# Optimization experiments

Measured on AMD Instinct MI355X. Metric: run time of the kernel, lower is better.

## Reference

```python
import jax, jax.numpy as jnp
import numpy as np

N, D = 768, 128  # num_cells, gnn embedding dim (sum(gnn_layers_out_chnls))

def setup_inputs() -> dict:
    key = jax.random.key(0)
    ks = jax.random.split(key, 5)
    z = jax.random.normal(ks[0], (N, D), dtype=jnp.float32)
    W1 = jax.random.normal(ks[1], (256, 2 * D), dtype=jnp.float32) * 0.05
    b1 = jnp.zeros((256,), dtype=jnp.float32)
    W2 = jax.random.normal(ks[2], (128, 256), dtype=jnp.float32) * 0.05
    b2 = jnp.zeros((128,), dtype=jnp.float32)
    Wf = jax.random.normal(ks[3], (2, 128), dtype=jnp.float32) * 0.05
    bf = jnp.zeros((2,), dtype=jnp.float32)
    return {"z": z, "W1": W1, "b1": b1, "W2": W2, "b2": b2, "Wf": Wf, "bf": bf}

def reference(z, W1, b1, W2, b2, Wf, bf):
    # pairs[i, j] = concat(z[j], z[i])  (rtile varies over j, ctile over i)
    # First 1x1 conv over the 2D-channel pair tensor is equivalent to two
    # small matmuls broadcast-summed (same math, avoids N*N*2D materialization).
    d = z.shape[1]
    row_part = jnp.einsum('jd,od->jo', z, W1[:, :d])   # contribution of z[j]
    col_part = jnp.einsum('id,od->io', z, W1[:, d:])   # contribution of z[i]
    h = jax.nn.relu(row_part[None, :, :] + col_part[:, None, :] + b1)  # [N, N, 256]
    # dropout is identity in eval mode (training=False)
    h = jax.nn.relu(jnp.einsum('ijc,oc->ijo', h, W2) + b2)             # [N, N, 128]
    dists = jnp.einsum('ijc,oc->ijo', h, Wf) + bf                      # [N, N, 2]
    return dists
```

## Files before the change

### kernel.cpp

```cpp
#include <hip/hip_runtime.h>


typedef __attribute__((ext_vector_type(8)))  _Float16     f16x8;
typedef __attribute__((ext_vector_type(2)))  float        f32x2;
typedef __attribute__((ext_vector_type(4)))  float        f32x4;
typedef __attribute__((ext_vector_type(16))) float        f32x16;

#define NCELL 768
#define DIM   128
#define C1    256
#define C2    128

#define CPB    0
#define CB     1024
#define WFT    3072
#define B2T    4096
#define LDS_SZ 4608

static __device__ __forceinline__ f32x2 pk_add(f32x2 a, f32x2 b) {
    f32x2 d; asm("v_pk_add_f32 %0, %1, %2" : "=v"(d) : "v"(a), "v"(b)); return d;
}
static __device__ __forceinline__ f32x2 pk_fma(f32x2 a, f32x2 b, f32x2 c) {
    f32x2 d; asm("v_pk_fma_f32 %0, %1, %2, %3" : "=v"(d) : "v"(a), "v"(b), "v"(c)); return d;
}
static __device__ __forceinline__ f32x2 relu2(f32x2 a) {
    f32x2 d; d[0] = fmaxf(a[0], 0.f); d[1] = fmaxf(a[1], 0.f); return d;
}
static __device__ __forceinline__ f32x2 lo2(f32x4 v) { return __builtin_shufflevector(v, v, 0, 1); }
static __device__ __forceinline__ f32x2 hi2(f32x4 v) { return __builtin_shufflevector(v, v, 2, 3); }

__global__ __launch_bounds__(256) void prep_all(const float* __restrict__ z,
                                                const float* __restrict__ W1,
                                                const float* __restrict__ b1,
                                                const float* __restrict__ W2,
                                                _Float16* __restrict__ rp16,
                                                _Float16* __restrict__ cp16,
                                                _Float16* __restrict__ w2h) {
    const int tid = threadIdx.x;
    if (blockIdx.x < 192) {
        const int jb4 = blockIdx.x * 4;
        __shared__ float zl[4 * DIM];
        zl[tid]       = z[(size_t)jb4 * DIM + tid];
        zl[tid + 256] = z[(size_t)jb4 * DIM + tid + 256];
        __syncthreads();
        const int o = tid;
        float a1[4] = {0.f, 0.f, 0.f, 0.f};
        float a2[4] = {0.f, 0.f, 0.f, 0.f};
        const f32x4* w4 = (const f32x4*)(W1 + (size_t)o * (2 * DIM));
#pragma unroll 4
        for (int d4 = 0; d4 < 32; ++d4) {
            f32x4 wa = w4[d4], wb = w4[32 + d4];
#pragma unroll
            for (int jj = 0; jj < 4; ++jj) {
                f32x4 zv = *(const f32x4*)(zl + jj * DIM + d4 * 4);
#pragma unroll
                for (int e = 0; e < 4; ++e) {
                    a1[jj] = fmaf(zv[e], wa[e], a1[jj]);
                    a2[jj] = fmaf(zv[e], wb[e], a2[jj]);
                }
            }
        }
        const float bb = b1[o];
#pragma unroll
        for (int jj = 0; jj < 4; ++jj) {
            rp16[(size_t)(jb4 + jj) * C1 + o] = (_Float16)(a1[jj] + bb);
            cp16[(size_t)(jb4 + jj) * C1 + o] = (_Float16)a2[jj];
        }
    } else {
        const int t = (blockIdx.x - 192) * 256 + tid;
        w2h[t] = (_Float16)W2[t];
    }
}

__global__ __launch_bounds__(256, 2) void pair_head(const _Float16* __restrict__ rp16,
                                                    const _Float16* __restrict__ cp16,
                                                    const _Float16* __restrict__ w2h,
                                                    const float* __restrict__ Wf,
                                                    const float* __restrict__ b2,
                                                    const float* __restrict__ bfv,
                                                    float* __restrict__ out) {
    __shared__ char smem[LDS_SZ];
    const int tid = threadIdx.x;
    const int nh  = tid >> 6;
    const int l   = tid & 63;
    const int ln  = l & 31;
    const int kh  = l >> 5;
    const int jbg = blockIdx.x >> 6;
    const int ic  = blockIdx.x & 63;
    const int j0  = jbg * 32;
    const int i_base = ic * 12;

    if (tid < 128) {
        int idx = tid >> 1, o = tid & 1;
        int kk = idx >> 5, q = (idx >> 2) & 7, ng = idx & 3;
        int r = 2 * q;
        int n0 = ng * 32 + (r & 3) + 8 * (r >> 2) + 4 * kk;
        f32x2 e = {Wf[o * C2 + n0], Wf[o * C2 + n0 + 1]};
        *(f32x2*)(smem + WFT + idx * 16 + o * 8) = e;
    }
    if (tid < 64) {
        int idx = tid;
        int kk = idx >> 5, q = (idx >> 2) & 7, ng = idx & 3;
        int r = 2 * q;
        int n0 = ng * 32 + (r & 3) + 8 * (r >> 2) + 4 * kk;
        f32x2 e = {b2[n0], b2[n0 + 1]};
        *(f32x2*)(smem + B2T + idx * 8) = e;
    }
    if (tid < 128) {
        unsigned v = *(const unsigned*)((const char*)cp16 + (size_t)i_base * 512 + tid * 4);
        *(unsigned*)(smem + CPB + tid * 4) = v;
    }

    f16x8 rpf[16];
    {
        const char* rsrc = (const char*)rp16 + (size_t)(j0 + ln) * 512 + kh * 16;
#pragma unroll
        for (int ks = 0; ks < 16; ++ks)
            rpf[ks] = *(const f16x8*)(rsrc + ks * 32);
    }
    f16x8 w2f[16];
#pragma unroll
    for (int ks = 0; ks < 16; ++ks)
        w2f[ks] = *(const f16x8*)(w2h + (size_t)(nh * 32 + ln) * C1 + ks * 16 + kh * 8);

    __syncthreads();

    const float bf0 = bfv[0], bf1 = bfv[1];
    const f16x8 zero8 = (f16x8)(_Float16)0.0f;

    for (int t = 0; t < 12; ++t) {
        unsigned cpv = 0;
        if (t < 11 && tid < 128)
            cpv = *(const unsigned*)((const char*)cp16 + (size_t)(i_base + t + 1) * 512 + tid * 4);

        const char* cbbase = smem + CPB + (t & 1) * 512 + kh * 16;

        f32x16 acc = (f32x16)0.f;
#pragma unroll
        for (int ks = 0; ks < 16; ++ks) {
            f16x8 cv = *(const f16x8*)(cbbase + ks * 32);
            f16x8 hb = __builtin_elementwise_max(rpf[ks] + cv, zero8);
            acc = __builtin_amdgcn_mfma_f32_32x32x16_f16(w2f[ks], hb, acc, 0, 0, 0);
        }

        f32x2 P0 = {0.f, 0.f}, P1 = {0.f, 0.f};
#pragma unroll
        for (int q = 0; q < 8; ++q) {
            int idx = kh * 32 + q * 4 + nh;
            f32x4 w01 = *(const f32x4*)(smem + WFT + idx * 16);
            f32x2 bb  = *(const f32x2*)(smem + B2T + idx * 8);
            f32x2 s = {acc[2 * q], acc[2 * q + 1]};
            s = relu2(pk_add(s, bb));
            P0 = pk_fma(lo2(w01), s, P0);
            P1 = pk_fma(hi2(w01), s, P1);
        }
        float p0 = P0[0] + P0[1], p1 = P1[0] + P1[1];
        p0 += __shfl_xor(p0, 32);
        p1 += __shfl_xor(p1, 32);
        if (kh == 0)
            *(f32x2*)(smem + CB + (t & 1) * 1024 + nh * 256 + ln * 8) = (f32x2){p0, p1};

        if (t < 11 && tid < 128)
            *(unsigned*)(smem + CPB + ((t + 1) & 1) * 512 + tid * 4) = cpv;

        __syncthreads();

        if (nh == (t & 3) && kh == 0) {
            const char* cbse = smem + CB + (t & 1) * 1024 + ln * 8;
            f32x2 a0 = *(const f32x2*)(cbse);
            f32x2 a1 = *(const f32x2*)(cbse + 256);
            f32x2 a2 = *(const f32x2*)(cbse + 512);
            f32x2 a3 = *(const f32x2*)(cbse + 768);
            float o0 = a0[0] + a1[0] + a2[0] + a3[0] + bf0;
            float o1 = a0[1] + a1[1] + a2[1] + a3[1] + bf1;
            const int i = i_base + t;
            *(f32x2*)(out + ((size_t)i * NCELL + j0 + ln) * 2) = (f32x2){o0, o1};
        }
    }
}

extern "C" void kernel_launch(void* const* d_in, const int* in_sizes, int n_in,
                              void* d_out, int out_size, void* d_ws, size_t ws_size,
                              hipStream_t stream) {
    const float* z   = (const float*)d_in[0];
    const float* W1  = (const float*)d_in[1];
    const float* b1  = (const float*)d_in[2];
    const float* W2  = (const float*)d_in[3];
    const float* b2  = (const float*)d_in[4];
    const float* Wf  = (const float*)d_in[5];
    const float* bfv = (const float*)d_in[6];
    float* out = (float*)d_out;

    _Float16* rp16 = (_Float16*)d_ws;
    _Float16* cp16 = rp16 + NCELL * C1;
    _Float16* w2h  = cp16 + NCELL * C1;

    prep_all<<<192 + 128, 256, 0, stream>>>(z, W1, b1, W2, rp16, cp16, w2h);
    pair_head<<<24 * 64, 256, 0, stream>>>(rp16, cp16, w2h, Wf, b2, bfv, out);
}
```

Baseline: 77.13 us.

## Switch pair head to 16x16x32 MFMA tiles with batched epilogue and single sync

Replaces the 32x32x16 MFMA per i-row with 16x16x32 MFMAs that process two i rows and two j halves at once, reusing each W2 and rp fragment across four products. The full block of 12 cp rows is staged into LDS up front, so the per-iteration double-buffered prefetch and the per-iteration __syncthreads go away. The Wf/b2 tables are packed into one table, and output reduction is deferred to a single pass after the loop. The cost is more accumulator registers and a larger LDS footprint, which could reduce occupancy.

Measured after the change: 64.04 us. 17.0% less time.

```diff
diff --git a/kernel.cpp b/kernel.cpp
--- a/kernel.cpp
+++ b/kernel.cpp
@@ -1,33 +1,21 @@
 #include <hip/hip_runtime.h>
 
 
-typedef __attribute__((ext_vector_type(8)))  _Float16     f16x8;
-typedef __attribute__((ext_vector_type(2)))  float        f32x2;
-typedef __attribute__((ext_vector_type(4)))  float        f32x4;
-typedef __attribute__((ext_vector_type(16))) float        f32x16;
+typedef __attribute__((ext_vector_type(8)))  _Float16 f16x8;
+typedef __attribute__((ext_vector_type(2)))  float    f32x2;
+typedef __attribute__((ext_vector_type(4)))  float    f32x4;
 
 #define NCELL 768
 #define DIM   128
 #define C1    256
 #define C2    128
 
-#define CPB    0
-#define CB     1024
-#define WFT    3072
-#define B2T    4096
-#define LDS_SZ 4608
-
-static __device__ __forceinline__ f32x2 pk_add(f32x2 a, f32x2 b) {
-    f32x2 d; asm("v_pk_add_f32 %0, %1, %2" : "=v"(d) : "v"(a), "v"(b)); return d;
-}
-static __device__ __forceinline__ f32x2 pk_fma(f32x2 a, f32x2 b, f32x2 c) {
-    f32x2 d; asm("v_pk_fma_f32 %0, %1, %2, %3" : "=v"(d) : "v"(a), "v"(b), "v"(c)); return d;
-}
-static __device__ __forceinline__ f32x2 relu2(f32x2 a) {
-    f32x2 d; d[0] = fmaxf(a[0], 0.f); d[1] = fmaxf(a[1], 0.f); return d;
-}
-static __device__ __forceinline__ f32x2 lo2(f32x4 v) { return __builtin_shufflevector(v, v, 0, 1); }
-static __device__ __forceinline__ f32x2 hi2(f32x4 v) { return __builtin_shufflevector(v, v, 2, 3); }
+#define CPL    0
+#define TAB    6144
+#define CBo    8192
+#define LDS_SZ 20480
+
+#define MFMA16(a, b, c) __builtin_amdgcn_mfma_f32_16x16x32_f16(a, b, c, 0, 0, 0)
 
 __global__ __launch_bounds__(256) void prep_all(const float* __restrict__ z,
                                                 const float* __restrict__ W1,
@@ -83,99 +71,114 @@
     const int tid = threadIdx.x;
     const int nh  = tid >> 6;
     const int l   = tid & 63;
-    const int ln  = l & 31;
-    const int kh  = l >> 5;
+    const int lc  = l & 15;
+    const int lg  = l >> 4;
     const int jbg = blockIdx.x >> 6;
     const int ic  = blockIdx.x & 63;
     const int j0  = jbg * 32;
     const int i_base = ic * 12;
 
+#pragma unroll
+    for (int q = 0; q < 6; ++q) {
+        int off = q * 256 + tid;
+        ((unsigned*)(smem + CPL))[off] =
+            ((const unsigned*)(cp16 + (size_t)i_base * C1))[off];
+    }
     if (tid < 128) {
-        int idx = tid >> 1, o = tid & 1;
-        int kk = idx >> 5, q = (idx >> 2) & 7, ng = idx & 3;
-        int r = 2 * q;
-        int n0 = ng * 32 + (r & 3) + 8 * (r >> 2) + 4 * kk;
-        f32x2 e = {Wf[o * C2 + n0], Wf[o * C2 + n0 + 1]};
-        *(f32x2*)(smem + WFT + idx * 16 + o * 8) = e;
-    }
-    if (tid < 64) {
-        int idx = tid;
-        int kk = idx >> 5, q = (idx >> 2) & 7, ng = idx & 3;
-        int r = 2 * q;
-        int n0 = ng * 32 + (r & 3) + 8 * (r >> 2) + 4 * kk;
-        f32x2 e = {b2[n0], b2[n0 + 1]};
-        *(f32x2*)(smem + B2T + idx * 8) = e;
-    }
-    if (tid < 128) {
-        unsigned v = *(const unsigned*)((const char*)cp16 + (size_t)i_base * 512 + tid * 4);
-        *(unsigned*)(smem + CPB + tid * 4) = v;
-    }
-
-    f16x8 rpf[16];
-    {
-        const char* rsrc = (const char*)rp16 + (size_t)(j0 + ln) * 512 + kh * 16;
-#pragma unroll
-        for (int ks = 0; ks < 16; ++ks)
-            rpf[ks] = *(const f16x8*)(rsrc + ks * 32);
-    }
-    f16x8 w2f[16];
-#pragma unroll
-    for (int ks = 0; ks < 16; ++ks)
-        w2f[ks] = *(const f16x8*)(w2h + (size_t)(nh * 32 + ln) * C1 + ks * 16 + kh * 8);
+        f32x4 e = {b2[tid], Wf[tid], Wf[C2 + tid], 0.f};
+        *(f32x4*)(smem + TAB + tid * 16) = e;
+    }
+
+    f16x8 rpf[2][8];
+#pragma unroll
+    for (int jh = 0; jh < 2; ++jh)
+#pragma unroll
+        for (int ks = 0; ks < 8; ++ks)
+            rpf[jh][ks] = *(const f16x8*)(rp16 + (size_t)(j0 + jh * 16 + lc) * C1 + lg * 8 + ks * 32);
+
+    f16x8 w2f[2][8];
+#pragma unroll
+    for (int ng = 0; ng < 2; ++ng)
+#pragma unroll
+        for (int ks = 0; ks < 8; ++ks)
+            w2f[ng][ks] = *(const f16x8*)(w2h + (size_t)(nh * 32 + ng * 16 + lc) * C1 + lg * 8 + ks * 32);
 
     __syncthreads();
 
+    const f16x8 z8 = (f16x8)(_Float16)0.0f;
+
+    for (int t = 0; t < 6; ++t) {
+        const char* c0 = smem + CPL + (2 * t) * 512 + lg * 16;
+
+        f32x4 a000 = (f32x4)0.f, a001 = (f32x4)0.f, a010 = (f32x4)0.f, a011 = (f32x4)0.f;
+        f32x4 a100 = (f32x4)0.f, a101 = (f32x4)0.f, a110 = (f32x4)0.f, a111 = (f32x4)0.f;
+
+#pragma unroll
+        for (int ks = 0; ks < 8; ++ks) {
+            f16x8 cv0 = *(const f16x8*)(c0 + ks * 64);
+            f16x8 cv1 = *(const f16x8*)(c0 + 512 + ks * 64);
+            f16x8 hb00 = __builtin_elementwise_max(rpf[0][ks] + cv0, z8);
+            f16x8 hb01 = __builtin_elementwise_max(rpf[1][ks] + cv0, z8);
+            f16x8 hb10 = __builtin_elementwise_max(rpf[0][ks] + cv1, z8);
+            f16x8 hb11 = __builtin_elementwise_max(rpf[1][ks] + cv1, z8);
+            a000 = MFMA16(w2f[0][ks], hb00, a000);
+            a001 = MFMA16(w2f[0][ks], hb01, a001);
+            a010 = MFMA16(w2f[0][ks], hb10, a010);
+            a011 = MFMA16(w2f[0][ks], hb11, a011);
+            a100 = MFMA16(w2f[1][ks], hb00, a100);
+            a101 = MFMA16(w2f[1][ks], hb01, a101);
+            a110 = MFMA16(w2f[1][ks], hb10, a110);
+            a111 = MFMA16(w2f[1][ks], hb11, a111);
+        }
+
+        f32x2 P00 = {0.f, 0.f}, P01 = {0.f, 0.f}, P10 = {0.f, 0.f}, P11 = {0.f, 0.f};
+#pragma unroll
+        for (int ng = 0; ng < 2; ++ng) {
+#pragma unroll
+            for (int r = 0; r < 4; ++r) {
+                int n = nh * 32 + ng * 16 + lg * 4 + r;
+                f32x4 e = *(const f32x4*)(smem + TAB + n * 16);
+                f32x4 q00 = ng ? a100 : a000, q01 = ng ? a101 : a001;
+                f32x4 q10 = ng ? a110 : a010, q11 = ng ? a111 : a011;
+                float h;
+                h = fmaxf(q00[r] + e[0], 0.f); P00[0] = fmaf(e[1], h, P00[0]); P00[1] = fmaf(e[2], h, P00[1]);
+                h = fmaxf(q01[r] + e[0], 0.f); P01[0] = fmaf(e[1], h, P01[0]); P01[1] = fmaf(e[2], h, P01[1]);
+                h = fmaxf(q10[r] + e[0], 0.f); P10[0] = fmaf(e[1], h, P10[0]); P10[1] = fmaf(e[2], h, P10[1]);
+                h = fmaxf(q11[r] + e[0], 0.f); P11[0] = fmaf(e[1], h, P11[0]); P11[1] = fmaf(e[2], h, P11[1]);
+            }
+        }
+#pragma unroll
+        for (int d = 16; d <= 32; d <<= 1) {
+            P00[0] += __shfl_xor(P00[0], d); P00[1] += __shfl_xor(P00[1], d);
+            P01[0] += __shfl_xor(P01[0], d); P01[1] += __shfl_xor(P01[1], d);
+            P10[0] += __shfl_xor(P10[0], d); P10[1] += __shfl_xor(P10[1], d);
+            P11[0] += __shfl_xor(P11[0], d); P11[1] += __shfl_xor(P11[1], d);
+        }
+        if (l < 16) {
+            char* cb = smem + CBo + (size_t)(t * 64 + l) * 32 + nh * 8;
+            *(f32x2*)(cb)           = P00;
+            *(f32x2*)(cb + 16 * 32) = P01;
+            *(f32x2*)(cb + 32 * 32) = P10;
+            *(f32x2*)(cb + 48 * 32) = P11;
+        }
+    }
+
+    __syncthreads();
+
     const float bf0 = bfv[0], bf1 = bfv[1];
-    const f16x8 zero8 = (f16x8)(_Float16)0.0f;
-
-    for (int t = 0; t < 12; ++t) {
-        unsigned cpv = 0;
-        if (t < 11 && tid < 128)
-            cpv = *(const unsigned*)((const char*)cp16 + (size_t)(i_base + t + 1) * 512 + tid * 4);
-
-        const char* cbbase = smem + CPB + (t & 1) * 512 + kh * 16;
-
-        f32x16 acc = (f32x16)0.f;
-#pragma unroll
-        for (int ks = 0; ks < 16; ++ks) {
-            f16x8 cv = *(const f16x8*)(cbbase + ks * 32);
-            f16x8 hb = __builtin_elementwise_max(rpf[ks] + cv, zero8);
-            acc = __builtin_amdgcn_mfma_f32_32x32x16_f16(w2f[ks], hb, acc, 0, 0, 0);
-        }
-
-        f32x2 P0 = {0.f, 0.f}, P1 = {0.f, 0.f};
-#pragma unroll
-        for (int q = 0; q < 8; ++q) {
-            int idx = kh * 32 + q * 4 + nh;
-            f32x4 w01 = *(const f32x4*)(smem + WFT + idx * 16);
-            f32x2 bb  = *(const f32x2*)(smem + B2T + idx * 8);
-            f32x2 s = {acc[2 * q], acc[2 * q + 1]};
-            s = relu2(pk_add(s, bb));
-            P0 = pk_fma(lo2(w01), s, P0);
-            P1 = pk_fma(hi2(w01), s, P1);
-        }
-        float p0 = P0[0] + P0[1], p1 = P1[0] + P1[1];
-        p0 += __shfl_xor(p0, 32);
-        p1 += __shfl_xor(p1, 32);
-        if (kh == 0)
-            *(f32x2*)(smem + CB + (t & 1) * 1024 + nh * 256 + ln * 8) = (f32x2){p0, p1};
-
-        if (t < 11 && tid < 128)
-            *(unsigned*)(smem + CPB + ((t + 1) & 1) * 512 + tid * 4) = cpv;
-
-        __syncthreads();
-
-        if (nh == (t & 3) && kh == 0) {
-            const char* cbse = smem + CB + (t & 1) * 1024 + ln * 8;
-            f32x2 a0 = *(const f32x2*)(cbse);
-            f32x2 a1 = *(const f32x2*)(cbse + 256);
-            f32x2 a2 = *(const f32x2*)(cbse + 512);
-            f32x2 a3 = *(const f32x2*)(cbse + 768);
-            float o0 = a0[0] + a1[0] + a2[0] + a3[0] + bf0;
-            float o1 = a0[1] + a1[1] + a2[1] + a3[1] + bf1;
-            const int i = i_base + t;
-            *(f32x2*)(out + ((size_t)i * NCELL + j0 + ln) * 2) = (f32x2){o0, o1};
-        }
+#pragma unroll
+    for (int p = tid; p < 384; p += 256) {
+        const char* cb = smem + CBo + (size_t)p * 32;
+        f32x2 a0 = *(const f32x2*)(cb);
+        f32x2 a1 = *(const f32x2*)(cb + 8);
+        f32x2 a2 = *(const f32x2*)(cb + 16);
+        f32x2 a3 = *(const f32x2*)(cb + 24);
+        float o0 = a0[0] + a1[0] + a2[0] + a3[0] + bf0;
+        float o1 = a0[1] + a1[1] + a2[1] + a3[1] + bf1;
+        int c = p & 15, jh = (p >> 4) & 1, ii = (p >> 5) & 1, t = p >> 6;
+        int i = i_base + 2 * t + ii;
+        int j = j0 + jh * 16 + c;
+        *(f32x2*)(out + ((size_t)i * NCELL + j) * 2) = (f32x2){o0, o1};
     }
 }
 
```
